# Optimization experiments

Hardware: AMD Instinct MI355X
Metric: run time of the kernel (lower is better)

Reference implementation:

```python
import jax, jax.numpy as jnp
import numpy as np

N, M, D, DV = 8192, 8192, 512, 512

def setup_inputs() -> dict:
    key = jax.random.key(0)
    kq, kk, kv = jax.random.split(key, 3)
    return {
        "query": jax.random.normal(kq, (N, D), dtype=jnp.float32),
        "key": jax.random.normal(kk, (M, D), dtype=jnp.float32),
        "value": jax.random.normal(kv, (M, DV), dtype=jnp.float32),
    }

def reference(query, key, value):
    # scores: [N, M] = Q @ K^T (no scale, no mask, matching the torch module)
    scores = query @ key.T
    attn = jax.nn.softmax(scores, axis=-1)
    return attn @ value
```

## Files before the change

### kernel.cpp

```cpp
#include <hip/hip_runtime.h>
#include <hip/hip_fp16.h>
#include <stdint.h>

typedef _Float16 f16;
typedef _Float16 f16x8 __attribute__((ext_vector_type(8)));
typedef float    f32x4 __attribute__((ext_vector_type(4)));
typedef int      i32x4 __attribute__((ext_vector_type(4)));

#define NQ 8192
#define NK 8192
#define DD 512
#define DVV 512

__device__ __forceinline__ void stage16(const void* g, void* ldsbase, int lane) {
#if __has_builtin(__builtin_amdgcn_global_load_lds)
  __builtin_amdgcn_global_load_lds((const __attribute__((address_space(1))) void*)g,
                                   (__attribute__((address_space(3))) void*)ldsbase, 16, 0, 0);
#else
  ((i32x4*)ldsbase)[lane] = *(const i32x4*)g;
#endif
}

__global__ void conv_hilo(const float* __restrict__ src, f16* __restrict__ hi,
                          f16* __restrict__ lo, int n8) {
  int i = blockIdx.x * 256 + threadIdx.x;
  if (i >= n8) return;
  const float4* s4 = (const float4*)src;
  float4 a = s4[2 * i], b = s4[2 * i + 1];
  float vv[8] = {a.x, a.y, a.z, a.w, b.x, b.y, b.z, b.w};
  f16 h8[8], l8[8];
#pragma unroll
  for (int j = 0; j < 8; ++j) {
    f16 h = (f16)vv[j];
    h8[j] = h;
    l8[j] = (f16)(vv[j] - (float)h);
  }
  *(f16x8*)(hi + (size_t)i * 8) = *(f16x8*)h8;
  *(f16x8*)(lo + (size_t)i * 8) = *(f16x8*)l8;
}

__global__ void conv_f16k(const float* __restrict__ src, f16* __restrict__ dst, int n8) {
  int i = blockIdx.x * 256 + threadIdx.x;
  if (i >= n8) return;
  const float4* s4 = (const float4*)src;
  float4 a = s4[2 * i], b = s4[2 * i + 1];
  float vv[8] = {a.x, a.y, a.z, a.w, b.x, b.y, b.z, b.w};
  f16 h8[8];
#pragma unroll
  for (int j = 0; j < 8; ++j) h8[j] = (f16)vv[j];
  *(f16x8*)(dst + (size_t)i * 8) = *(f16x8*)h8;
}

__global__ void conv_vT(const float* __restrict__ v, f16* __restrict__ vT) {
  __shared__ float t[64][65];
  int k0 = blockIdx.x * 64, d0 = blockIdx.y * 64;
#pragma unroll
  for (int e = 0; e < 16; ++e) {
    int idx = threadIdx.x + e * 256;
    int kr = idx >> 6, dc = idx & 63;
    t[kr][dc] = v[(size_t)(k0 + kr) * DVV + d0 + dc];
  }
  __syncthreads();
  int dl = threadIdx.x >> 2, seg = (threadIdx.x & 3) * 16;
  f16 tmp[16];
#pragma unroll
  for (int c = 0; c < 16; ++c) tmp[c] = (f16)t[seg + c][dl];
  f16* dst = vT + (size_t)(d0 + dl) * NK + k0 + seg;
  *(f16x8*)dst = *(f16x8*)tmp;
  *(f16x8*)(dst + 8) = *(f16x8*)(tmp + 8);
}

__global__ __launch_bounds__(256, 3) void qk_kernel(
    const f16* __restrict__ qhi, const f16* __restrict__ qlo,
    const f16* __restrict__ khi,
    f16* __restrict__ s16, float* __restrict__ pm, float* __restrict__ ps) {
  __shared__ f16 ls0[128 * 64];
  __shared__ f16 ls1[128 * 64];
  __shared__ f16 ls2[128 * 64];
  __shared__ float red[2][2][64];
  const int tid = threadIdx.x;
  const int lane = tid & 63, wid = tid >> 6;
  const int wr = wid >> 1, wc = wid & 1;
  const int bx = blockIdx.x, by = blockIdx.y;
  const int lo16 = lane & 15, hi4 = lane >> 4;

  f32x4 acc[4][4] = {};

  const f16* qa = qhi + (size_t)(by * 128) * DD;
  const f16* qb = qlo + (size_t)(by * 128) * DD;
  const f16* ka = khi + (size_t)(bx * 128) * DD;
  const int srw = lane >> 3;
  const int sc = (lane & 7) ^ srw;

  for (int dt = 0; dt < 8; ++dt) {
    __syncthreads();
#pragma unroll
    for (int u = wid; u < 48; u += 4) {
      int t = u >> 4, rb8 = u & 15;
      int row = rb8 * 8 + srw;
      const f16* src = (t == 0 ? qa : (t == 1 ? qb : ka)) + (size_t)row * DD + dt * 64 + sc * 8;
      f16* dst = (t == 0 ? ls0 : (t == 1 ? ls1 : ls2)) + rb8 * 512;
      stage16(src, dst, lane);
    }
    __syncthreads();
#pragma unroll
    for (int ks = 0; ks < 2; ++ks) {
      f16x8 ah[4], al[4], bh[4];
#pragma unroll
      for (int i = 0; i < 4; ++i) {
        int row = wr * 64 + i * 16 + lo16;
        int off = row * 64 + (((ks * 4 + hi4) ^ (row & 7)) << 3);
        ah[i] = *(const f16x8*)&ls0[off];
        al[i] = *(const f16x8*)&ls1[off];
      }
#pragma unroll
      for (int j = 0; j < 4; ++j) {
        int row = wc * 64 + j * 16 + lo16;
        int off = row * 64 + (((ks * 4 + hi4) ^ (row & 7)) << 3);
        bh[j] = *(const f16x8*)&ls2[off];
      }
#pragma unroll
      for (int i = 0; i < 4; ++i)
#pragma unroll
        for (int j = 0; j < 4; ++j) {
          acc[i][j] = __builtin_amdgcn_mfma_f32_16x16x32_f16(ah[i], bh[j], acc[i][j], 0, 0, 0);
          acc[i][j] = __builtin_amdgcn_mfma_f32_16x16x32_f16(al[i], bh[j], acc[i][j], 0, 0, 0);
        }
    }
  }

  float rmax[4][4];
#pragma unroll
  for (int i = 0; i < 4; ++i)
#pragma unroll
    for (int r = 0; r < 4; ++r) {
      float m = fmaxf(fmaxf(acc[i][0][r], acc[i][1][r]), fmaxf(acc[i][2][r], acc[i][3][r]));
#pragma unroll
      for (int d = 1; d < 16; d <<= 1) m = fmaxf(m, __shfl_xor(m, d, 64));
      rmax[i][r] = m;
    }
  __syncthreads();
  if (lo16 == 0) {
#pragma unroll
    for (int i = 0; i < 4; ++i)
#pragma unroll
      for (int r = 0; r < 4; ++r) red[wr][wc][i * 16 + hi4 * 4 + r] = rmax[i][r];
  }
  __syncthreads();
  float pmv[4][4];
#pragma unroll
  for (int i = 0; i < 4; ++i)
#pragma unroll
    for (int r = 0; r < 4; ++r) {
      int rl = i * 16 + hi4 * 4 + r;
      pmv[i][r] = fmaxf(red[wr][0][rl], red[wr][1][rl]);
    }
  __syncthreads();
  float rsum[4][4];
#pragma unroll
  for (int i = 0; i < 4; ++i)
#pragma unroll
    for (int r = 0; r < 4; ++r) {
      float s = 0.f;
#pragma unroll
      for (int j = 0; j < 4; ++j) {
        float p = __expf(acc[i][j][r] - pmv[i][r]);
        acc[i][j][r] = p;
        s += p;
      }
#pragma unroll
      for (int d = 1; d < 16; d <<= 1) s += __shfl_xor(s, d, 64);
      rsum[i][r] = s;
    }
#pragma unroll
  for (int i = 0; i < 4; ++i)
#pragma unroll
    for (int r = 0; r < 4; ++r) {
      size_t grow = (size_t)(by * 128 + wr * 64 + i * 16 + hi4 * 4 + r);
#pragma unroll
      for (int j = 0; j < 4; ++j)
        s16[grow * NK + bx * 128 + wc * 64 + j * 16 + lo16] = (f16)acc[i][j][r];
    }
  if (lo16 == 0) {
#pragma unroll
    for (int i = 0; i < 4; ++i)
#pragma unroll
      for (int r = 0; r < 4; ++r) red[wr][wc][i * 16 + hi4 * 4 + r] = rsum[i][r];
  }
  __syncthreads();
  if (wc == 0 && lo16 == 0) {
#pragma unroll
    for (int i = 0; i < 4; ++i)
#pragma unroll
      for (int r = 0; r < 4; ++r) {
        int rl = i * 16 + hi4 * 4 + r;
        size_t grow = (size_t)(by * 128 + wr * 64 + rl);
        pm[grow * 64 + bx] = pmv[i][r];
        ps[grow * 64 + bx] = red[wr][0][rl] + red[wr][1][rl];
      }
  }
}

__global__ void red_kernel(const float* __restrict__ pm, const float* __restrict__ ps,
                           float* __restrict__ coef) {
  int row = blockIdx.x * 4 + (threadIdx.x >> 6);
  int t = threadIdx.x & 63;
  float pmt = pm[(size_t)row * 64 + t];
  float m = pmt;
#pragma unroll
  for (int d = 1; d < 64; d <<= 1) m = fmaxf(m, __shfl_xor(m, d, 64));
  float e = __expf(pmt - m);
  float l = ps[(size_t)row * 64 + t] * e;
#pragma unroll
  for (int d = 1; d < 64; d <<= 1) l += __shfl_xor(l, d, 64);
  coef[(size_t)row * 64 + t] = e / l;
}

__global__ __launch_bounds__(256, 2) void pv_kernel(
    const f16* __restrict__ p16, const float* __restrict__ coef,
    const f16* __restrict__ vT, float* __restrict__ dst,
    int steps, size_t zstride) {
  __shared__ f16 lsA[2][128 * 64];
  __shared__ f16 lsB[2][128 * 64];
  const int tid = threadIdx.x, lane = tid & 63, wid = tid >> 6;
  const int lo16 = lane & 15, hi4 = lane >> 4;
  const int wr = wid >> 1, wc = wid & 1;
  const int bx = blockIdx.x, by = blockIdx.y, bz = blockIdx.z;
  const int g0 = bz * steps;
  f32x4 acc[4][4] = {};

  const int arow0 = tid >> 3, acol = tid & 7;
  const int srw = lane >> 3;
  const int sc = (lane & 7) ^ srw;

  f16x8 va[4];
  float scv[4];

#pragma unroll
  for (int u = 0; u < 4; ++u)
    va[u] = *(const f16x8*)(p16 + (size_t)(by * 128 + u * 32 + arow0) * NK + (size_t)g0 * 64 + acol * 8);
#pragma unroll
  for (int i = 0; i < 4; ++i) {
    int unit = wid * 4 + i;
    int row = unit * 8 + srw;
    stage16(vT + (size_t)(bx * 128 + row) * NK + (size_t)g0 * 64 + sc * 8,
            &lsB[0][unit * 512], lane);
  }
#pragma unroll
  for (int u = 0; u < 4; ++u)
    scv[u] = coef[(size_t)(by * 128 + u * 32 + arow0) * 64 + (g0 >> 1)];
#pragma unroll
  for (int u = 0; u < 4; ++u) {
    int row = u * 32 + arow0;
    f16x8 vv = va[u] * (f16)scv[u];
    *(f16x8*)&lsA[0][row * 64 + ((acol ^ (row & 7)) << 3)] = vv;
  }
  __syncthreads();

  for (int s = 0; s < steps; ++s) {
    const int cur = s & 1, nxt = cur ^ 1;
    const int g = g0 + s;
    if (s + 1 < steps) {
#pragma unroll
      for (int u = 0; u < 4; ++u)
        va[u] = *(const f16x8*)(p16 + (size_t)(by * 128 + u * 32 + arow0) * NK +
                                (size_t)(g + 1) * 64 + acol * 8);
#pragma unroll
      for (int i = 0; i < 4; ++i) {
        int unit = wid * 4 + i;
        int row = unit * 8 + srw;
        stage16(vT + (size_t)(bx * 128 + row) * NK + (size_t)(g + 1) * 64 + sc * 8,
                &lsB[nxt][unit * 512], lane);
      }
#pragma unroll
      for (int u = 0; u < 4; ++u)
        scv[u] = coef[(size_t)(by * 128 + u * 32 + arow0) * 64 + ((g + 1) >> 1)];
    }
#pragma unroll
    for (int ks = 0; ks < 2; ++ks) {
      f16x8 af[4], bf[4];
#pragma unroll
      for (int i = 0; i < 4; ++i) {
        int row = wr * 64 + i * 16 + lo16;
        af[i] = *(const f16x8*)&lsA[cur][row * 64 + (((ks * 4 + hi4) ^ (row & 7)) << 3)];
      }
#pragma unroll
      for (int j = 0; j < 4; ++j) {
        int dv = wc * 64 + j * 16 + lo16;
        bf[j] = *(const f16x8*)&lsB[cur][dv * 64 + (((ks * 4 + hi4) ^ (dv & 7)) << 3)];
      }
#pragma unroll
      for (int i = 0; i < 4; ++i)
#pragma unroll
        for (int j = 0; j < 4; ++j)
          acc[i][j] = __builtin_amdgcn_mfma_f32_16x16x32_f16(af[i], bf[j], acc[i][j], 0, 0, 0);
    }
    if (s + 1 < steps) {
#pragma unroll
      for (int u = 0; u < 4; ++u) {
        int row = u * 32 + arow0;
        f16x8 vv = va[u] * (f16)scv[u];
        *(f16x8*)&lsA[nxt][row * 64 + ((acol ^ (row & 7)) << 3)] = vv;
      }
    }
    __syncthreads();
  }

  float* o = dst + (size_t)bz * zstride;
#pragma unroll
  for (int i = 0; i < 4; ++i)
#pragma unroll
    for (int j = 0; j < 4; ++j)
#pragma unroll
      for (int r = 0; r < 4; ++r)
        o[(size_t)(by * 128 + wr * 64 + i * 16 + hi4 * 4 + r) * DVV +
          bx * 128 + wc * 64 + j * 16 + lo16] = acc[i][j][r];
}

__global__ void reduce_out(const float* __restrict__ part, float* __restrict__ out,
                           int ks, size_t n4) {
  size_t i = (size_t)blockIdx.x * 256 + threadIdx.x;
  if (i >= n4) return;
  float4 a = ((const float4*)part)[i];
  for (int z = 1; z < ks; ++z) {
    float4 b = ((const float4*)(part + z * n4 * 4))[i];
    a.x += b.x; a.y += b.y; a.z += b.z; a.w += b.w;
  }
  ((float4*)out)[i] = a;
}

__global__ void zero_out(float* o, int n) {
  int i = blockIdx.x * 256 + threadIdx.x;
  if (i < n) o[i] = 0.f;
}

extern "C" void kernel_launch(void* const* d_in, const int* in_sizes, int n_in,
                              void* d_out, int out_size, void* d_ws, size_t ws_size,
                              hipStream_t stream) {
  (void)in_sizes; (void)n_in; (void)out_size;
  const float* Q = (const float*)d_in[0];
  const float* K = (const float*)d_in[1];
  const float* V = (const float*)d_in[2];
  float* out = (float*)d_out;

  const size_t sz16 = (size_t)NK * DD * 2;
  const size_t fixedB = 2 * sz16;
  const size_t perRow = 1024 * 2 + 256 * 3 + (size_t)NK * 2;
  const size_t partB = (size_t)16384 * DVV * 4;
  int nc = 0;
  for (int cand = 8192; cand >= 1024; cand >>= 1)
    if (fixedB + (size_t)cand * perRow + partB <= ws_size) { nc = cand; break; }
  if (nc == 0) {
    zero_out<<<(NQ * DVV + 255) / 256, 256, 0, stream>>>(out, NQ * DVV);
    return;
  }
  const int ks = 16384 / nc;
  const int steps = 128 / ks;

  char* w = (char*)d_ws;
  f16* khi = (f16*)w;
  f16* vT = (f16*)(w + sz16);
  char* p = w + fixedB;
  f16* qhi = (f16*)p;      p += (size_t)nc * 1024;
  f16* qlo = (f16*)p;      p += (size_t)nc * 1024;
  float* pm = (float*)p;   p += (size_t)nc * 256;
  float* ps = (float*)p;   p += (size_t)nc * 256;
  float* coef = (float*)p; p += (size_t)nc * 256;
  f16* s16 = (f16*)p;      p += (size_t)nc * NK * 2;
  float* part = (float*)p;

  conv_f16k<<<NK * DD / 8 / 256, 256, 0, stream>>>(K, khi, NK * DD / 8);
  conv_vT<<<dim3(NK / 64, DVV / 64), 256, 0, stream>>>(V, vT);

  for (int c = 0; c < NQ / nc; ++c) {
    conv_hilo<<<nc * DD / 8 / 256, 256, 0, stream>>>(Q + (size_t)c * nc * DD, qhi, qlo, nc * DD / 8);
    qk_kernel<<<dim3(NK / 128, nc / 128), 256, 0, stream>>>(qhi, qlo, khi, s16, pm, ps);
    red_kernel<<<nc / 4, 256, 0, stream>>>(pm, ps, coef);
    pv_kernel<<<dim3(DVV / 128, nc / 128, ks), 256, 0, stream>>>(
        s16, coef, vT, part, steps, (size_t)nc * DVV);
    reduce_out<<<(int)(((size_t)nc * DVV / 4 + 255) / 256), 256, 0, stream>>>(
        part, out + (size_t)c * nc * DVV, ks, (size_t)nc * DVV / 4);
  }
}
```

Measured before the change: 303.7 us.

## Enlarge QK tile to 256x256 with triple-buffered async LDS staging

The QK^T kernel now uses 512 threads on a 256x256 output tile instead of 128x128. The D loop runs in 32-wide slices through a three-stage LDS ring fed by direct global-to-LDS loads, with explicit vmcnt waits, barriers and s_setprio around the MFMA bursts. This is meant to raise operand reuse, overlap global loads with matrix math, and cut the number of per-block partial softmax statistics. Because those partials drop from 64 to 32 per row, the reduction kernel and the PV coefficient indexing change to match. The costs are higher register pressure (32 accumulator tiles per wave), about 144KB of LDS per block, and fragile hand-managed synchronisation.

```diff
diff --git a/kernel.cpp b/kernel.cpp
--- a/kernel.cpp
+++ b/kernel.cpp
@@ -70,68 +70,109 @@
   *(f16x8*)(dst + 8) = *(f16x8*)(tmp + 8);
 }
 
-__global__ __launch_bounds__(256, 3) void qk_kernel(
+__global__ __launch_bounds__(512, 2) void qk_kernel(
     const f16* __restrict__ qhi, const f16* __restrict__ qlo,
     const f16* __restrict__ khi,
     f16* __restrict__ s16, float* __restrict__ pm, float* __restrict__ ps) {
-  __shared__ f16 ls0[128 * 64];
-  __shared__ f16 ls1[128 * 64];
-  __shared__ f16 ls2[128 * 64];
-  __shared__ float red[2][2][64];
+  __shared__ f16 LS[3 * 3 * 8192];
+  __shared__ float red[2][4][128];
   const int tid = threadIdx.x;
   const int lane = tid & 63, wid = tid >> 6;
-  const int wr = wid >> 1, wc = wid & 1;
+  const int wr = wid >> 2, wc = wid & 3;
   const int bx = blockIdx.x, by = blockIdx.y;
   const int lo16 = lane & 15, hi4 = lane >> 4;
-
-  f32x4 acc[4][4] = {};
-
-  const f16* qa = qhi + (size_t)(by * 128) * DD;
-  const f16* qb = qlo + (size_t)(by * 128) * DD;
-  const f16* ka = khi + (size_t)(bx * 128) * DD;
-  const int srw = lane >> 3;
-  const int sc = (lane & 7) ^ srw;
-
-  for (int dt = 0; dt < 8; ++dt) {
-    __syncthreads();
-#pragma unroll
-    for (int u = wid; u < 48; u += 4) {
-      int t = u >> 4, rb8 = u & 15;
-      int row = rb8 * 8 + srw;
-      const f16* src = (t == 0 ? qa : (t == 1 ? qb : ka)) + (size_t)row * DD + dt * 64 + sc * 8;
-      f16* dst = (t == 0 ? ls0 : (t == 1 ? ls1 : ls2)) + rb8 * 512;
-      stage16(src, dst, lane);
-    }
-    __syncthreads();
-#pragma unroll
-    for (int ks = 0; ks < 2; ++ks) {
-      f16x8 ah[4], al[4], bh[4];
-#pragma unroll
-      for (int i = 0; i < 4; ++i) {
-        int row = wr * 64 + i * 16 + lo16;
-        int off = row * 64 + (((ks * 4 + hi4) ^ (row & 7)) << 3);
-        ah[i] = *(const f16x8*)&ls0[off];
-        al[i] = *(const f16x8*)&ls1[off];
-      }
+  const int swz = (lo16 & 3) ^ ((lo16 >> 2) & 3);
+  const int u_s = hi4 ^ swz;
+
+  f32x4 acc[8][4] = {};
+
+  const f16* tp[3] = {qhi + (size_t)(by * 256) * DD, qlo + (size_t)(by * 256) * DD,
+                      khi + (size_t)(bx * 256) * DD};
+  const int srow4 = lane >> 2, usl = lane & 3;
+  const f16* sptr[6];
+  int dbase[6];
+#pragma unroll
+  for (int s2 = 0; s2 < 6; ++s2) {
+    int u = wid + s2 * 8;
+    int tt = u >> 4, rb = u & 15;
+    int r = rb * 16 + srow4;
+    int ug = usl ^ (r & 3) ^ ((r >> 2) & 3);
+    sptr[s2] = tp[tt] + (size_t)r * DD + ug * 8;
+    dbase[s2] = tt * 3 * 8192 + rb * 512;
+  }
+  f16* lsf = (f16*)LS;
+
+#define STG(s2, t2, buf) stage16(sptr[s2] + (t2) * 32, lsf + dbase[s2] + (buf) * 8192, lane)
+
+#pragma unroll
+  for (int s2 = 0; s2 < 6; ++s2) STG(s2, 0, 0);
+#pragma unroll
+  for (int s2 = 0; s2 < 6; ++s2) STG(s2, 1, 1);
+  asm volatile("s_waitcnt vmcnt(6)" ::: "memory");
+  __builtin_amdgcn_s_barrier();
+  asm volatile("" ::: "memory");
+
+  const int abase = (wr * 128 + lo16) * 32 + u_s * 8;
+  const int bbase = (wc * 64 + lo16) * 32 + u_s * 8;
+
+  int cur = 0, pre = 2;
+  for (int t = 0; t < 16; ++t) {
+    const f16* Qh = lsf + cur * 8192;
+    const f16* Ql = lsf + (3 + cur) * 8192;
+    const f16* Kh = lsf + (6 + cur) * 8192;
+    const bool st = (t <= 13);
+    f16x8 bfr[4], ah[4], al[4];
+#pragma unroll
+    for (int j = 0; j < 4; ++j) bfr[j] = *(const f16x8*)&Kh[bbase + j * 512];
+#pragma unroll
+    for (int i = 0; i < 4; ++i) {
+      ah[i] = *(const f16x8*)&Qh[abase + i * 512];
+      al[i] = *(const f16x8*)&Ql[abase + i * 512];
+    }
+    if (st) { STG(0, t + 2, pre); STG(1, t + 2, pre); STG(2, t + 2, pre); }
+    __builtin_amdgcn_s_barrier();
+    asm volatile("" ::: "memory");
+    __builtin_amdgcn_s_setprio(1);
+#pragma unroll
+    for (int i = 0; i < 4; ++i)
 #pragma unroll
       for (int j = 0; j < 4; ++j) {
-        int row = wc * 64 + j * 16 + lo16;
-        int off = row * 64 + (((ks * 4 + hi4) ^ (row & 7)) << 3);
-        bh[j] = *(const f16x8*)&ls2[off];
-      }
-#pragma unroll
-      for (int i = 0; i < 4; ++i)
-#pragma unroll
-        for (int j = 0; j < 4; ++j) {
-          acc[i][j] = __builtin_amdgcn_mfma_f32_16x16x32_f16(ah[i], bh[j], acc[i][j], 0, 0, 0);
-          acc[i][j] = __builtin_amdgcn_mfma_f32_16x16x32_f16(al[i], bh[j], acc[i][j], 0, 0, 0);
-        }
-    }
-  }
-
-  float rmax[4][4];
-#pragma unroll
-  for (int i = 0; i < 4; ++i)
+        acc[i][j] = __builtin_amdgcn_mfma_f32_16x16x32_f16(ah[i], bfr[j], acc[i][j], 0, 0, 0);
+        acc[i][j] = __builtin_amdgcn_mfma_f32_16x16x32_f16(al[i], bfr[j], acc[i][j], 0, 0, 0);
+      }
+    __builtin_amdgcn_s_setprio(0);
+    __builtin_amdgcn_s_barrier();
+    asm volatile("" ::: "memory");
+#pragma unroll
+    for (int i = 0; i < 4; ++i) {
+      ah[i] = *(const f16x8*)&Qh[abase + (4 + i) * 512];
+      al[i] = *(const f16x8*)&Ql[abase + (4 + i) * 512];
+    }
+    if (st) { STG(3, t + 2, pre); STG(4, t + 2, pre); STG(5, t + 2, pre); }
+    __builtin_amdgcn_s_barrier();
+    asm volatile("" ::: "memory");
+    __builtin_amdgcn_s_setprio(1);
+#pragma unroll
+    for (int i = 0; i < 4; ++i)
+#pragma unroll
+      for (int j = 0; j < 4; ++j) {
+        acc[4 + i][j] = __builtin_amdgcn_mfma_f32_16x16x32_f16(ah[i], bfr[j], acc[4 + i][j], 0, 0, 0);
+        acc[4 + i][j] = __builtin_amdgcn_mfma_f32_16x16x32_f16(al[i], bfr[j], acc[4 + i][j], 0, 0, 0);
+      }
+    __builtin_amdgcn_s_setprio(0);
+    if (st) asm volatile("s_waitcnt vmcnt(6)" ::: "memory");
+    else    asm volatile("s_waitcnt vmcnt(0)" ::: "memory");
+    __builtin_amdgcn_s_barrier();
+    asm volatile("" ::: "memory");
+    cur = (cur == 2) ? 0 : cur + 1;
+    pre = (pre == 2) ? 0 : pre + 1;
+  }
+#undef STG
+
+  __syncthreads();
+  float rmax[8][4];
+#pragma unroll
+  for (int i = 0; i < 8; ++i)
 #pragma unroll
     for (int r = 0; r < 4; ++r) {
       float m = fmaxf(fmaxf(acc[i][0][r], acc[i][1][r]), fmaxf(acc[i][2][r], acc[i][3][r]));
@@ -139,26 +180,26 @@
       for (int d = 1; d < 16; d <<= 1) m = fmaxf(m, __shfl_xor(m, d, 64));
       rmax[i][r] = m;
     }
-  __syncthreads();
   if (lo16 == 0) {
 #pragma unroll
-    for (int i = 0; i < 4; ++i)
+    for (int i = 0; i < 8; ++i)
 #pragma unroll
       for (int r = 0; r < 4; ++r) red[wr][wc][i * 16 + hi4 * 4 + r] = rmax[i][r];
   }
   __syncthreads();
-  float pmv[4][4];
-#pragma unroll
-  for (int i = 0; i < 4; ++i)
+  float pmv[8][4];
+#pragma unroll
+  for (int i = 0; i < 8; ++i)
 #pragma unroll
     for (int r = 0; r < 4; ++r) {
       int rl = i * 16 + hi4 * 4 + r;
-      pmv[i][r] = fmaxf(red[wr][0][rl], red[wr][1][rl]);
-    }
-  __syncthreads();
-  float rsum[4][4];
-#pragma unroll
-  for (int i = 0; i < 4; ++i)
+      pmv[i][r] = fmaxf(fmaxf(red[wr][0][rl], red[wr][1][rl]),
+                        fmaxf(red[wr][2][rl], red[wr][3][rl]));
+    }
+  __syncthreads();
+  float rsum[8][4];
+#pragma unroll
+  for (int i = 0; i < 8; ++i)
 #pragma unroll
     for (int r = 0; r < 4; ++r) {
       float s = 0.f;
@@ -173,47 +214,47 @@
       rsum[i][r] = s;
     }
 #pragma unroll
-  for (int i = 0; i < 4; ++i)
+  for (int i = 0; i < 8; ++i)
 #pragma unroll
     for (int r = 0; r < 4; ++r) {
-      size_t grow = (size_t)(by * 128 + wr * 64 + i * 16 + hi4 * 4 + r);
+      size_t grow = (size_t)(by * 256 + wr * 128 + i * 16 + hi4 * 4 + r);
 #pragma unroll
       for (int j = 0; j < 4; ++j)
-        s16[grow * NK + bx * 128 + wc * 64 + j * 16 + lo16] = (f16)acc[i][j][r];
+        s16[grow * NK + bx * 256 + wc * 64 + j * 16 + lo16] = (f16)acc[i][j][r];
     }
   if (lo16 == 0) {
 #pragma unroll
-    for (int i = 0; i < 4; ++i)
+    for (int i = 0; i < 8; ++i)
 #pragma unroll
       for (int r = 0; r < 4; ++r) red[wr][wc][i * 16 + hi4 * 4 + r] = rsum[i][r];
   }
   __syncthreads();
   if (wc == 0 && lo16 == 0) {
 #pragma unroll
-    for (int i = 0; i < 4; ++i)
+    for (int i = 0; i < 8; ++i)
 #pragma unroll
       for (int r = 0; r < 4; ++r) {
         int rl = i * 16 + hi4 * 4 + r;
-        size_t grow = (size_t)(by * 128 + wr * 64 + rl);
-        pm[grow * 64 + bx] = pmv[i][r];
-        ps[grow * 64 + bx] = red[wr][0][rl] + red[wr][1][rl];
+        size_t grow = (size_t)(by * 256 + wr * 128 + rl);
+        pm[grow * 32 + bx] = pmv[i][r];
+        ps[grow * 32 + bx] = red[wr][0][rl] + red[wr][1][rl] + red[wr][2][rl] + red[wr][3][rl];
       }
   }
 }
 
 __global__ void red_kernel(const float* __restrict__ pm, const float* __restrict__ ps,
                            float* __restrict__ coef) {
-  int row = blockIdx.x * 4 + (threadIdx.x >> 6);
-  int t = threadIdx.x & 63;
-  float pmt = pm[(size_t)row * 64 + t];
+  int row = blockIdx.x * 8 + (threadIdx.x >> 5);
+  int t = threadIdx.x & 31;
+  float pmt = pm[(size_t)row * 32 + t];
   float m = pmt;
 #pragma unroll
-  for (int d = 1; d < 64; d <<= 1) m = fmaxf(m, __shfl_xor(m, d, 64));
+  for (int d = 1; d < 32; d <<= 1) m = fmaxf(m, __shfl_xor(m, d, 32));
   float e = __expf(pmt - m);
-  float l = ps[(size_t)row * 64 + t] * e;
-#pragma unroll
-  for (int d = 1; d < 64; d <<= 1) l += __shfl_xor(l, d, 64);
-  coef[(size_t)row * 64 + t] = e / l;
+  float l = ps[(size_t)row * 32 + t] * e;
+#pragma unroll
+  for (int d = 1; d < 32; d <<= 1) l += __shfl_xor(l, d, 32);
+  coef[(size_t)row * 32 + t] = e / l;
 }
 
 __global__ __launch_bounds__(256, 2) void pv_kernel(
@@ -248,7 +289,7 @@
   }
 #pragma unroll
   for (int u = 0; u < 4; ++u)
-    scv[u] = coef[(size_t)(by * 128 + u * 32 + arow0) * 64 + (g0 >> 1)];
+    scv[u] = coef[(size_t)(by * 128 + u * 32 + arow0) * 32 + (g0 >> 2)];
 #pragma unroll
   for (int u = 0; u < 4; ++u) {
     int row = u * 32 + arow0;
@@ -274,7 +315,7 @@
       }
 #pragma unroll
       for (int u = 0; u < 4; ++u)
-        scv[u] = coef[(size_t)(by * 128 + u * 32 + arow0) * 64 + ((g + 1) >> 1)];
+        scv[u] = coef[(size_t)(by * 128 + u * 32 + arow0) * 32 + ((g + 1) >> 2)];
     }
 #pragma unroll
     for (int ks = 0; ks < 2; ++ks) {
@@ -345,7 +386,7 @@
 
   const size_t sz16 = (size_t)NK * DD * 2;
   const size_t fixedB = 2 * sz16;
-  const size_t perRow = 1024 * 2 + 256 * 3 + (size_t)NK * 2;
+  const size_t perRow = 1024 * 2 + 128 * 3 + (size_t)NK * 2;
   const size_t partB = (size_t)16384 * DVV * 4;
   int nc = 0;
   for (int cand = 8192; cand >= 1024; cand >>= 1)
@@ -363,9 +404,9 @@
   char* p = w + fixedB;
   f16* qhi = (f16*)p;      p += (size_t)nc * 1024;
   f16* qlo = (f16*)p;      p += (size_t)nc * 1024;
-  float* pm = (float*)p;   p += (size_t)nc * 256;
-  float* ps = (float*)p;   p += (size_t)nc * 256;
-  float* coef = (float*)p; p += (size_t)nc * 256;
+  float* pm = (float*)p;   p += (size_t)nc * 128;
+  float* ps = (float*)p;   p += (size_t)nc * 128;
+  float* coef = (float*)p; p += (size_t)nc * 128;
   f16* s16 = (f16*)p;      p += (size_t)nc * NK * 2;
   float* part = (float*)p;
 
@@ -374,8 +415,8 @@
 
   for (int c = 0; c < NQ / nc; ++c) {
     conv_hilo<<<nc * DD / 8 / 256, 256, 0, stream>>>(Q + (size_t)c * nc * DD, qhi, qlo, nc * DD / 8);
-    qk_kernel<<<dim3(NK / 128, nc / 128), 256, 0, stream>>>(qhi, qlo, khi, s16, pm, ps);
-    red_kernel<<<nc / 4, 256, 0, stream>>>(pm, ps, coef);
+    qk_kernel<<<dim3(NK / 256, nc / 256), 512, 0, stream>>>(qhi, qlo, khi, s16, pm, ps);
+    red_kernel<<<nc / 8, 256, 0, stream>>>(pm, ps, coef);
     pv_kernel<<<dim3(DVV / 128, nc / 128, ks), 256, 0, stream>>>(
         s16, coef, vT, part, steps, (size_t)nc * DVV);
     reduce_out<<<(int)(((size_t)nc * DVV / 4 + 255) / 256), 256, 0, stream>>>(
```

Result: no change. 303.5 us (-0.0%).

## Drop Q hi/lo split, double-buffer QK staging, coalesce score stores via LDS

Applied to the files above, without the earlier changes.

Converts Q to a single fp16 copy instead of hi/lo halves, which halves the MFMA work in the QK kernel. The QK main loop gets double-buffered LDS staging with one barrier per step and raised priority around the MFMAs. Exponentiated scores are written through swizzled LDS so global stores are 16-byte vectors. The chunking logic now prefers one full-size chunk with no split-K for PV, removing the partial-sum reduction. The trade-off is lower precision in the score computation.

```diff
diff --git a/kernel.cpp b/kernel.cpp
--- a/kernel.cpp
+++ b/kernel.cpp
@@ -11,6 +11,7 @@
 #define NK 8192
 #define DD 512
 #define DVV 512
+#define LOG2E 1.44269504f
 
 __device__ __forceinline__ void stage16(const void* g, void* ldsbase, int lane) {
 #if __has_builtin(__builtin_amdgcn_global_load_lds)
@@ -21,24 +22,6 @@
 #endif
 }
 
-__global__ void conv_hilo(const float* __restrict__ src, f16* __restrict__ hi,
-                          f16* __restrict__ lo, int n8) {
-  int i = blockIdx.x * 256 + threadIdx.x;
-  if (i >= n8) return;
-  const float4* s4 = (const float4*)src;
-  float4 a = s4[2 * i], b = s4[2 * i + 1];
-  float vv[8] = {a.x, a.y, a.z, a.w, b.x, b.y, b.z, b.w};
-  f16 h8[8], l8[8];
-#pragma unroll
-  for (int j = 0; j < 8; ++j) {
-    f16 h = (f16)vv[j];
-    h8[j] = h;
-    l8[j] = (f16)(vv[j] - (float)h);
-  }
-  *(f16x8*)(hi + (size_t)i * 8) = *(f16x8*)h8;
-  *(f16x8*)(lo + (size_t)i * 8) = *(f16x8*)l8;
-}
-
 __global__ void conv_f16k(const float* __restrict__ src, f16* __restrict__ dst, int n8) {
   int i = blockIdx.x * 256 + threadIdx.x;
   if (i >= n8) return;
@@ -70,64 +53,79 @@
   *(f16x8*)(dst + 8) = *(f16x8*)(tmp + 8);
 }
 
-__global__ __launch_bounds__(256, 3) void qk_kernel(
-    const f16* __restrict__ qhi, const f16* __restrict__ qlo,
-    const f16* __restrict__ khi,
+__global__ __launch_bounds__(256, 2) void qk_kernel(
+    const f16* __restrict__ q16, const f16* __restrict__ k16,
     f16* __restrict__ s16, float* __restrict__ pm, float* __restrict__ ps) {
-  __shared__ f16 ls0[128 * 64];
-  __shared__ f16 ls1[128 * 64];
-  __shared__ f16 ls2[128 * 64];
+  __shared__ f16 LS[2 * 2 * 8192];
   __shared__ float red[2][2][64];
-  const int tid = threadIdx.x;
-  const int lane = tid & 63, wid = tid >> 6;
+  const int tid = threadIdx.x, lane = tid & 63, wid = tid >> 6;
   const int wr = wid >> 1, wc = wid & 1;
   const int bx = blockIdx.x, by = blockIdx.y;
   const int lo16 = lane & 15, hi4 = lane >> 4;
 
   f32x4 acc[4][4] = {};
 
-  const f16* qa = qhi + (size_t)(by * 128) * DD;
-  const f16* qb = qlo + (size_t)(by * 128) * DD;
-  const f16* ka = khi + (size_t)(bx * 128) * DD;
-  const int srw = lane >> 3;
-  const int sc = (lane & 7) ^ srw;
-
-  for (int dt = 0; dt < 8; ++dt) {
-    __syncthreads();
-#pragma unroll
-    for (int u = wid; u < 48; u += 4) {
-      int t = u >> 4, rb8 = u & 15;
-      int row = rb8 * 8 + srw;
-      const f16* src = (t == 0 ? qa : (t == 1 ? qb : ka)) + (size_t)row * DD + dt * 64 + sc * 8;
-      f16* dst = (t == 0 ? ls0 : (t == 1 ? ls1 : ls2)) + rb8 * 512;
-      stage16(src, dst, lane);
-    }
-    __syncthreads();
-#pragma unroll
-    for (int ks = 0; ks < 2; ++ks) {
-      f16x8 ah[4], al[4], bh[4];
-#pragma unroll
-      for (int i = 0; i < 4; ++i) {
-        int row = wr * 64 + i * 16 + lo16;
-        int off = row * 64 + (((ks * 4 + hi4) ^ (row & 7)) << 3);
-        ah[i] = *(const f16x8*)&ls0[off];
-        al[i] = *(const f16x8*)&ls1[off];
-      }
-#pragma unroll
-      for (int j = 0; j < 4; ++j) {
-        int row = wc * 64 + j * 16 + lo16;
-        int off = row * 64 + (((ks * 4 + hi4) ^ (row & 7)) << 3);
-        bh[j] = *(const f16x8*)&ls2[off];
-      }
-#pragma unroll
-      for (int i = 0; i < 4; ++i)
-#pragma unroll
-        for (int j = 0; j < 4; ++j) {
-          acc[i][j] = __builtin_amdgcn_mfma_f32_16x16x32_f16(ah[i], bh[j], acc[i][j], 0, 0, 0);
-          acc[i][j] = __builtin_amdgcn_mfma_f32_16x16x32_f16(al[i], bh[j], acc[i][j], 0, 0, 0);
-        }
-    }
-  }
+  const int srw = lane >> 3, sc8 = (lane & 7) ^ srw;
+  const f16* sptr[8];
+  int dbase[8];
+#pragma unroll
+  for (int s = 0; s < 8; ++s) {
+    int u = wid + s * 4;
+    int tt = u >> 4, rb = u & 15;
+    int row = rb * 8 + srw;
+    sptr[s] = (tt == 0 ? q16 + (size_t)(by * 128 + row) * DD
+                       : k16 + (size_t)(bx * 128 + row) * DD) + sc8 * 8;
+    dbase[s] = tt * 8192 + rb * 512;
+  }
+#define STG(t2, buf)                                                     \
+  do {                                                                   \
+    _Pragma("unroll") for (int s = 0; s < 8; ++s)                        \
+        stage16(sptr[s] + (t2) * 64, LS + (buf) * 16384 + dbase[s], lane); \
+  } while (0)
+
+  int aoff[4][2], boff[4][2];
+#pragma unroll
+  for (int m = 0; m < 4; ++m)
+#pragma unroll
+    for (int kk = 0; kk < 2; ++kk) {
+      int row = wr * 64 + m * 16 + lo16;
+      aoff[m][kk] = row * 64 + (((kk * 4 + hi4) ^ (row & 7)) << 3);
+      int rowb = wc * 64 + m * 16 + lo16;
+      boff[m][kk] = 8192 + rowb * 64 + (((kk * 4 + hi4) ^ (rowb & 7)) << 3);
+    }
+
+  STG(0, 0);
+  asm volatile("s_waitcnt vmcnt(0)" ::: "memory");
+  __builtin_amdgcn_s_barrier();
+  asm volatile("" ::: "memory");
+
+  for (int t = 0; t < 8; ++t) {
+    const int cur = t & 1;
+    if (t < 7) STG(t + 1, cur ^ 1);
+    const f16* Bb = LS + cur * 16384;
+    f16x8 af[4][2], bf[2][4];
+#pragma unroll
+    for (int n = 0; n < 4; ++n)
+#pragma unroll
+      for (int kk = 0; kk < 2; ++kk) bf[kk][n] = *(const f16x8*)&Bb[boff[n][kk]];
+#pragma unroll
+    for (int m = 0; m < 4; ++m)
+#pragma unroll
+      for (int kk = 0; kk < 2; ++kk) af[m][kk] = *(const f16x8*)&Bb[aoff[m][kk]];
+    __builtin_amdgcn_s_setprio(1);
+#pragma unroll
+    for (int m = 0; m < 4; ++m)
+#pragma unroll
+      for (int n = 0; n < 4; ++n) {
+        acc[m][n] = __builtin_amdgcn_mfma_f32_16x16x32_f16(af[m][0], bf[0][n], acc[m][n], 0, 0, 0);
+        acc[m][n] = __builtin_amdgcn_mfma_f32_16x16x32_f16(af[m][1], bf[1][n], acc[m][n], 0, 0, 0);
+      }
+    __builtin_amdgcn_s_setprio(0);
+    asm volatile("s_waitcnt vmcnt(0)" ::: "memory");
+    __builtin_amdgcn_s_barrier();
+    asm volatile("" ::: "memory");
+  }
+#undef STG
 
   float rmax[4][4];
 #pragma unroll
@@ -139,7 +137,6 @@
       for (int d = 1; d < 16; d <<= 1) m = fmaxf(m, __shfl_xor(m, d, 64));
       rmax[i][r] = m;
     }
-  __syncthreads();
   if (lo16 == 0) {
 #pragma unroll
     for (int i = 0; i < 4; ++i)
@@ -161,25 +158,18 @@
   for (int i = 0; i < 4; ++i)
 #pragma unroll
     for (int r = 0; r < 4; ++r) {
+      int qloc = wr * 64 + i * 16 + hi4 * 4 + r;
       float s = 0.f;
 #pragma unroll
       for (int j = 0; j < 4; ++j) {
-        float p = __expf(acc[i][j][r] - pmv[i][r]);
-        acc[i][j][r] = p;
+        float p = exp2f((acc[i][j][r] - pmv[i][r]) * LOG2E);
         s += p;
+        int kloc = wc * 64 + j * 16 + lo16;
+        LS[qloc * 128 + (((kloc >> 3) ^ (qloc & 7)) << 3) + (kloc & 7)] = (f16)p;
       }
 #pragma unroll
       for (int d = 1; d < 16; d <<= 1) s += __shfl_xor(s, d, 64);
       rsum[i][r] = s;
-    }
-#pragma unroll
-  for (int i = 0; i < 4; ++i)
-#pragma unroll
-    for (int r = 0; r < 4; ++r) {
-      size_t grow = (size_t)(by * 128 + wr * 64 + i * 16 + hi4 * 4 + r);
-#pragma unroll
-      for (int j = 0; j < 4; ++j)
-        s16[grow * NK + bx * 128 + wc * 64 + j * 16 + lo16] = (f16)acc[i][j][r];
     }
   if (lo16 == 0) {
 #pragma unroll
@@ -198,6 +188,17 @@
         pm[grow * 64 + bx] = pmv[i][r];
         ps[grow * 64 + bx] = red[wr][0][rl] + red[wr][1][rl];
       }
+  }
+  {
+    const int q = tid >> 1, half = tid & 1;
+    f16* gdst = s16 + (size_t)(by * 128 + q) * NK + bx * 128 + half * 64;
+    const int sw = (q & 7) << 3;
+#pragma unroll
+    for (int e = 0; e < 8; ++e) {
+      int k0 = half * 64 + e * 8;
+      f16x8 v = *(const f16x8*)&LS[q * 128 + (((k0 >> 3) << 3) ^ sw)];
+      *(f16x8*)(gdst + e * 8) = v;
+    }
   }
 }
 
@@ -209,7 +210,7 @@
   float m = pmt;
 #pragma unroll
   for (int d = 1; d < 64; d <<= 1) m = fmaxf(m, __shfl_xor(m, d, 64));
-  float e = __expf(pmt - m);
+  float e = exp2f((pmt - m) * LOG2E);
   float l = ps[(size_t)row * 64 + t] * e;
 #pragma unroll
   for (int d = 1; d < 64; d <<= 1) l += __shfl_xor(l, d, 64);
@@ -345,40 +346,47 @@
 
   const size_t sz16 = (size_t)NK * DD * 2;
   const size_t fixedB = 2 * sz16;
-  const size_t perRow = 1024 * 2 + 256 * 3 + (size_t)NK * 2;
-  const size_t partB = (size_t)16384 * DVV * 4;
-  int nc = 0;
-  for (int cand = 8192; cand >= 1024; cand >>= 1)
-    if (fixedB + (size_t)cand * perRow + partB <= ws_size) { nc = cand; break; }
+  const size_t perRow = 1024 + 64 * 4 * 3 + (size_t)NK * 2;
+  const size_t partB = (size_t)8192 * DVV * 4;
+  int nc = 0, ks = 1;
+  if (fixedB + 8192 * perRow <= ws_size) {
+    nc = 8192; ks = 1;
+  } else {
+    for (int cand = 4096; cand >= 1024; cand >>= 1)
+      if (fixedB + (size_t)cand * perRow + partB <= ws_size) { nc = cand; ks = 8192 / cand; break; }
+  }
   if (nc == 0) {
     zero_out<<<(NQ * DVV + 255) / 256, 256, 0, stream>>>(out, NQ * DVV);
     return;
   }
-  const int ks = 16384 / nc;
   const int steps = 128 / ks;
 
   char* w = (char*)d_ws;
-  f16* khi = (f16*)w;
+  f16* k16 = (f16*)w;
   f16* vT = (f16*)(w + sz16);
   char* p = w + fixedB;
-  f16* qhi = (f16*)p;      p += (size_t)nc * 1024;
-  f16* qlo = (f16*)p;      p += (size_t)nc * 1024;
+  f16* q16 = (f16*)p;      p += (size_t)nc * 1024;
   float* pm = (float*)p;   p += (size_t)nc * 256;
   float* ps = (float*)p;   p += (size_t)nc * 256;
   float* coef = (float*)p; p += (size_t)nc * 256;
   f16* s16 = (f16*)p;      p += (size_t)nc * NK * 2;
   float* part = (float*)p;
 
-  conv_f16k<<<NK * DD / 8 / 256, 256, 0, stream>>>(K, khi, NK * DD / 8);
+  conv_f16k<<<NK * DD / 8 / 256, 256, 0, stream>>>(K, k16, NK * DD / 8);
   conv_vT<<<dim3(NK / 64, DVV / 64), 256, 0, stream>>>(V, vT);
 
   for (int c = 0; c < NQ / nc; ++c) {
-    conv_hilo<<<nc * DD / 8 / 256, 256, 0, stream>>>(Q + (size_t)c * nc * DD, qhi, qlo, nc * DD / 8);
-    qk_kernel<<<dim3(NK / 128, nc / 128), 256, 0, stream>>>(qhi, qlo, khi, s16, pm, ps);
+    conv_f16k<<<nc * DD / 8 / 256, 256, 0, stream>>>(Q + (size_t)c * nc * DD, q16, nc * DD / 8);
+    qk_kernel<<<dim3(NK / 128, nc / 128), 256, 0, stream>>>(q16, k16, s16, pm, ps);
     red_kernel<<<nc / 4, 256, 0, stream>>>(pm, ps, coef);
-    pv_kernel<<<dim3(DVV / 128, nc / 128, ks), 256, 0, stream>>>(
-        s16, coef, vT, part, steps, (size_t)nc * DVV);
-    reduce_out<<<(int)(((size_t)nc * DVV / 4 + 255) / 256), 256, 0, stream>>>(
-        part, out + (size_t)c * nc * DVV, ks, (size_t)nc * DVV / 4);
-  }
-}
+    if (ks == 1) {
+      pv_kernel<<<dim3(DVV / 128, nc / 128, 1), 256, 0, stream>>>(
+          s16, coef, vT, out + (size_t)c * nc * DVV, steps, 0);
+    } else {
+      pv_kernel<<<dim3(DVV / 128, nc / 128, ks), 256, 0, stream>>>(
+          s16, coef, vT, part, steps, (size_t)nc * DVV);
+      reduce_out<<<(int)(((size_t)nc * DVV / 4 + 255) / 256), 256, 0, stream>>>(
+          part, out + (size_t)c * nc * DVV, ks, (size_t)nc * DVV / 4);
+    }
+  }
+}
```

Measured after the change: 353.3 us. +16.4%, slower.
